# Performance work log

Measured on AMD Instinct MI355X. Metric: run time of the kernel, lower is better.

## Reference

```python
import jax, jax.numpy as jnp
import numpy as np

H, D = 8, 16
HD = H * D
SCALE0 = float(1.0 / np.sqrt(D * 1))   # degree-0 dot-product scale (order m=1)
SCALE1 = float(1.0 / np.sqrt(D * 3))   # degree-1 dot-product scale (order m=3)
SHARED = float(np.sqrt(0.5))           # shared_scale = sqrt(1/2) for DOT_PROD + SHARED
NEG = -1e9


def _split_heads_q(x):  # (b,n,HD,m) -> (b,H,n,D,m)
    b, n, _, m = x.shape
    return x.reshape(b, n, H, D, m).transpose(0, 2, 1, 3, 4)


def _split_heads_k(x):  # (b,n,N,HD,m) -> (b,H,n,N,D,m)
    b, n, N, _, m = x.shape
    return x.reshape(b, n, N, H, D, m).transpose(0, 3, 1, 2, 4, 5)


def _augment_kv(k, v, feats, W_self, null_k, null_v):
    # attend_self: VNLinear self key/value; use_null_kv: learned null tokens.
    b, n = feats.shape[:2]
    m = feats.shape[-1]
    skv = jnp.einsum('oc,bncm->bnom', W_self, feats)          # (b,n,2HD,m)
    sk, sv = jnp.split(skv, 2, axis=-2)
    sk = _split_heads_q(sk)[:, :, :, None]                     # (b,H,n,1,D,m)
    sv = _split_heads_q(sv)[:, :, :, None]
    nk = jnp.broadcast_to(null_k[None, :, None, None], (b, H, n, 1, D, m))
    nv = jnp.broadcast_to(null_v[None, :, None, None], (b, H, n, 1, D, m))
    k = jnp.concatenate([nk, sk, k], axis=3)                   # (b,H,n,2+N,D,m)
    v = jnp.concatenate([nv, sv, v], axis=3)
    return k, v


def _merge_heads(x):  # (b,H,n,D,m) -> (b,n,HD,m)
    b, _, n, _, m = x.shape
    return x.transpose(0, 2, 1, 3, 4).reshape(b, n, HD, m)


def _forward(q0, k0, v0, q1, k1, v1, feats0, feats1, edges,
             W_self_kv0, W_self_kv1, W_bias, self_bias, null_bias,
             null_k0, null_v0, null_k1, null_v1, head_weights1,
             W_out0, W_out1, neighbor_mask):
    b, n, N = edges.shape[:3]
    q0h, k0h, v0h = _split_heads_q(q0), _split_heads_k(k0), _split_heads_k(v0)
    q1h, k1h, v1h = _split_heads_q(q1), _split_heads_k(k1), _split_heads_k(v1)
    k0h, v0h = _augment_kv(k0h, v0h, feats0, W_self_kv0, null_k0, null_v0)
    k1h, v1h = _augment_kv(k1h, v1h, feats1, W_self_kv1, null_k1, null_v1)

    # pair bias for degree 0 (to_order==1); prepend null/self bias columns
    edge_bias = jnp.einsum('bnje,he->bhnj', edges, W_bias)     # (b,H,n,N)
    nb = jnp.broadcast_to(null_bias[None, :, None, None], (b, H, n, 1))
    sb = jnp.broadcast_to(self_bias[None, :, None, None], (b, H, n, 1))
    bias = jnp.concatenate([nb, sb, edge_bias], axis=-1)        # (b,H,n,2+N)

    sim0 = jnp.einsum('bhndm,bhnjdm->bhnj', q0h, k0h) * SCALE0 + bias
    w1 = jax.nn.softplus(head_weights1)                         # (1,H,1,1)
    sim1 = jnp.einsum('bhndm,bhnjdm->bhnj', q1h, k1h) * (SCALE1 * w1)

    total = (sim0 + sim1) * SHARED
    mask = jnp.concatenate(
        [jnp.ones((b, 1, n, 2), dtype=bool),                    # null + self always valid
         neighbor_mask[:, None]], axis=-1)
    total = jnp.where(mask, total, NEG)
    attn = jax.nn.softmax(total, axis=-1)                       # shared across degrees

    out0 = _merge_heads(jnp.einsum('bhnj,bhnjdm->bhndm', attn, v0h))
    out1 = _merge_heads(jnp.einsum('bhnj,bhnjdm->bhndm', attn, v1h))

    y0 = jnp.einsum('oc,bncm->bnom', W_out0, out0)              # FiberLinear deg 0
    y1 = jnp.einsum('oc,bncm->bnom', W_out1, out1)              # FiberLinear deg 1
    return y0, y1


def setup_inputs() -> dict:
    key = jax.random.key(0)
    ks = jax.random.split(key, 20)
    b, n, N, e = 1, 2048, 32, 32
    d0, d1 = 128, 64
    f = lambda k, s: jax.random.normal(k, s, dtype=jnp.float32) * 0.1
    return {
        'q0': f(ks[0], (b, n, HD, 1)), 'k0': f(ks[1], (b, n, N, HD, 1)), 'v0': f(ks[2], (b, n, N, HD, 1)),
        'q1': f(ks[3], (b, n, HD, 3)), 'k1': f(ks[4], (b, n, N, HD, 3)), 'v1': f(ks[5], (b, n, N, HD, 3)),
        'feats0': f(ks[6], (b, n, d0, 1)), 'feats1': f(ks[7], (b, n, d1, 3)),
        'edges': f(ks[8], (b, n, N, e)),
        'W_self_kv0': f(ks[9], (2 * HD, d0)), 'W_self_kv1': f(ks[10], (2 * HD, d1)),
        'W_bias': f(ks[11], (H, e)),
        'self_bias': jnp.zeros((H,), jnp.float32), 'null_bias': jnp.zeros((H,), jnp.float32),
        'null_k0': jnp.zeros((H, D, 1), jnp.float32), 'null_v0': jnp.zeros((H, D, 1), jnp.float32),
        'null_k1': jnp.zeros((H, D, 3), jnp.float32), 'null_v1': jnp.zeros((H, D, 3), jnp.float32),
        'head_weights1': jnp.full((1, H, 1, 1), float(np.log(np.e - 1.0)), jnp.float32),
        'W_out0': f(ks[12], (d0, HD)), 'W_out1': f(ks[13], (d1, HD)),
        'neighbor_mask': jax.random.uniform(ks[14], (b, n, N)) > 0.1,
    }


def reference(q0, k0, v0, q1, k1, v1, feats0, feats1, edges,
              W_self_kv0, W_self_kv1, W_bias, self_bias, null_bias,
              null_k0, null_v0, null_k1, null_v1, head_weights1,
              W_out0, W_out1, neighbor_mask):
    return _forward(q0, k0, v0, q1, k1, v1, feats0, feats1, edges,
                    W_self_kv0, W_self_kv1, W_bias, self_bias, null_bias,
                    null_k0, null_v0, null_k1, null_v1, head_weights1,
                    W_out0, W_out1, neighbor_mask)
```

## Files before the change

kernel.cpp:

```cpp
#include <hip/hip_runtime.h>

constexpr int kH  = 8;
constexpr int kD  = 16;
constexpr int kHD = 128;
constexpr int kN  = 32;
constexpr int kE  = 32;
constexpr int kD0 = 128;
constexpr int kD1 = 64;
constexpr int kP  = 4;
constexpr int kP3 = 2;
constexpr int kPP = 8;

constexpr float SCALE0   = 0.25f;
constexpr float SCALE1   = 0.14433756729740643f;
constexpr float SHARED_S = 0.70710678118654752f;
constexpr float NEGV     = -1e9f;


__global__ __launch_bounds__(256) void k1_selfkv(
    const float* __restrict__ q0, const float* __restrict__ q1,
    const float* __restrict__ feats0, const float* __restrict__ feats1,
    const float* __restrict__ Wskv0, const float* __restrict__ Wskv1,
    const float* __restrict__ self_bias, const float* __restrict__ null_bias,
    const float* __restrict__ nk0, const float* __restrict__ nk1,
    const float* __restrict__ hw1,
    float* __restrict__ ws_sc, float* __restrict__ ws_sv0, float* __restrict__ ws_sv1)
{
  const int i0 = blockIdx.x * kP;
  const int t  = threadIdx.x;
  __shared__ __align__(16) float f0s[kP][kD0];
  __shared__ __align__(16) float f1s[kP][kD1 * 3];
  __shared__ __align__(16) float q0s[kP][kHD];
  __shared__ __align__(16) float q1s[kP][kHD * 3];
  __shared__ float sk0L[kP][kHD];
  __shared__ float sk1L[kP][kHD * 3];
  __shared__ float w1s[kH];

  for (int u = t; u < kP * 32; u += 256) { int p = u >> 5, r = u & 31;
    ((float4*)f0s[p])[r] = ((const float4*)(feats0 + (size_t)(i0 + p) * kD0))[r]; }
  for (int u = t; u < kP * 48; u += 256) { int p = u / 48, r = u % 48;
    ((float4*)f1s[p])[r] = ((const float4*)(feats1 + (size_t)(i0 + p) * kD1 * 3))[r]; }
  for (int u = t; u < kP * 32; u += 256) { int p = u >> 5, r = u & 31;
    ((float4*)q0s[p])[r] = ((const float4*)(q0 + (size_t)(i0 + p) * kHD))[r]; }
  for (int u = t; u < kP * 96; u += 256) { int p = u / 96, r = u % 96;
    ((float4*)q1s[p])[r] = ((const float4*)(q1 + (size_t)(i0 + p) * kHD * 3))[r]; }
  if (t < kH) w1s[t] = log1pf(expf(hw1[t]));
  __syncthreads();

  float acc0[kP] = {};
  {
    const float4* wr = (const float4*)(Wskv0 + t * kD0);
    #pragma unroll
    for (int g = 0; g < 32; ++g) {
      float4 w = wr[g]; int c = g * 4;
      #pragma unroll
      for (int p = 0; p < kP; ++p)
        acc0[p] += w.x * f0s[p][c] + w.y * f0s[p][c + 1]
                 + w.z * f0s[p][c + 2] + w.w * f0s[p][c + 3];
    }
  }
  float acc1[kP][3] = {};
  {
    const float4* wr = (const float4*)(Wskv1 + t * kD1);
    #pragma unroll
    for (int g = 0; g < 16; ++g) {
      float4 w = wr[g]; int c = g * 4;
      float wv[4] = {w.x, w.y, w.z, w.w};
      #pragma unroll
      for (int q = 0; q < 4; ++q) {
        #pragma unroll
        for (int p = 0; p < kP; ++p) {
          const float* fp = &f1s[p][(c + q) * 3];
          acc1[p][0] += wv[q] * fp[0];
          acc1[p][1] += wv[q] * fp[1];
          acc1[p][2] += wv[q] * fp[2];
        }
      }
    }
  }
  if (t < kHD) {
    #pragma unroll
    for (int p = 0; p < kP; ++p) {
      sk0L[p][t] = acc0[p];
      sk1L[p][t * 3 + 0] = acc1[p][0];
      sk1L[p][t * 3 + 1] = acc1[p][1];
      sk1L[p][t * 3 + 2] = acc1[p][2];
    }
  } else {
    const int o = t - kHD;
    #pragma unroll
    for (int p = 0; p < kP; ++p) {
      ws_sv0[(size_t)(i0 + p) * kHD + o] = acc0[p];
      float* sp = ws_sv1 + (size_t)(i0 + p) * kHD * 3 + o * 3;
      sp[0] = acc1[p][0]; sp[1] = acc1[p][1]; sp[2] = acc1[p][2];
    }
  }
  __syncthreads();

  if (t < kP * 16) {
    const int p = t >> 4, idx = t & 15;
    const int h = idx & 7;
    const bool is_self = idx >= 8;
    float s0 = 0.f, s1 = 0.f, bias;
    if (is_self) {
      #pragma unroll
      for (int d = 0; d < kD; ++d) s0 += q0s[p][h * kD + d] * sk0L[p][h * kD + d];
      #pragma unroll
      for (int x = 0; x < 48; ++x) s1 += q1s[p][h * 48 + x] * sk1L[p][h * 48 + x];
      bias = self_bias[h];
    } else {
      #pragma unroll
      for (int d = 0; d < kD; ++d) s0 += q0s[p][h * kD + d] * nk0[h * kD + d];
      #pragma unroll
      for (int x = 0; x < 48; ++x) s1 += q1s[p][h * 48 + x] * nk1[h * 48 + x];
      bias = null_bias[h];
    }
    float total = (s0 * SCALE0 + bias + s1 * SCALE1 * w1s[h]) * SHARED_S;
    ws_sc[(size_t)(i0 + p) * 272 + h * 34 + (is_self ? 1 : 0)] = total;
  }
}

__global__ __launch_bounds__(256) void k2_sims(
    const float* __restrict__ q0, const float* __restrict__ q1,
    const float* __restrict__ k0, const float* __restrict__ k1,
    const float* __restrict__ edges, const float* __restrict__ Wbias,
    const float* __restrict__ hw1, const int* __restrict__ nmask,
    float* __restrict__ ws_sc)
{
  const int i = blockIdx.x;
  const int t = threadIdx.x;
  __shared__ __align__(16) float q0s[kHD];
  __shared__ __align__(16) float q1s[kHD * 3];
  __shared__ __align__(16) float edg[kN][kE + 1];
  __shared__ float wbs[kH * kE];
  __shared__ float w1s[kH];

  if (t < 32) {
    ((float4*)q0s)[t] = ((const float4*)(q0 + (size_t)i * kHD))[t];
  } else if (t < 128) {
    int r = t - 32;
    ((float4*)q1s)[r] = ((const float4*)(q1 + (size_t)i * kHD * 3))[r];
  }
  {
    float4 v = ((const float4*)(edges + (size_t)i * kN * kE))[t];
    int j = t >> 3, e4 = (t & 7) * 4;
    float* dst = &edg[j][e4];
    dst[0] = v.x; dst[1] = v.y; dst[2] = v.z; dst[3] = v.w;
  }
  if (t < kH * kE) wbs[t] = Wbias[t];
  if (t < kH) w1s[t] = log1pf(expf(hw1[t]));
  __syncthreads();

  const int h = t >> 5, j = t & 31;

  float bias = 0.f;
  #pragma unroll
  for (int e = 0; e < kE; ++e) bias += edg[j][e] * wbs[h * kE + e];

  float s0 = 0.f;
  const float4* kr0 = (const float4*)(k0 + ((size_t)i * kN + j) * kHD + h * kD);
  #pragma unroll
  for (int g = 0; g < 4; ++g) {
    float4 w = kr0[g]; int x = h * kD + g * 4;
    s0 += w.x * q0s[x] + w.y * q0s[x + 1] + w.z * q0s[x + 2] + w.w * q0s[x + 3];
  }
  float s1 = 0.f;
  const float4* kr1 = (const float4*)(k1 + ((size_t)i * kN + j) * kHD * 3 + h * 48);
  #pragma unroll
  for (int g = 0; g < 12; ++g) {
    float4 w = kr1[g]; int x = h * 48 + g * 4;
    s1 += w.x * q1s[x] + w.y * q1s[x + 1] + w.z * q1s[x + 2] + w.w * q1s[x + 3];
  }

  float total = (s0 * SCALE0 + bias + s1 * SCALE1 * w1s[h]) * SHARED_S;
  bool valid = nmask[(size_t)i * kN + j] != 0;
  float sc = valid ? total : NEGV;

  float* row = ws_sc + (size_t)i * 272 + h * 34;
  float e0v = row[0], e1v = row[1];

  float mx = sc;
  #pragma unroll
  for (int off = 16; off > 0; off >>= 1) mx = fmaxf(mx, __shfl_xor(mx, off));
  mx = fmaxf(mx, fmaxf(e0v, e1v));
  float ex = __expf(sc - mx);
  float sum = ex;
  #pragma unroll
  for (int off = 16; off > 0; off >>= 1) sum += __shfl_xor(sum, off);
  float ee0 = __expf(e0v - mx), ee1 = __expf(e1v - mx);
  float inv = 1.f / (sum + ee0 + ee1);

  row[2 + j] = ex * inv;
  if (j == 0) row[0] = ee0 * inv;
  if (j == 1) row[1] = ee1 * inv;
}

__global__ __launch_bounds__(256, 4) void k3_accum(
    const float* __restrict__ v0, const float* __restrict__ v1,
    const float* __restrict__ nv0, const float* __restrict__ nv1,
    const float* __restrict__ ws_sc,
    float* __restrict__ ws_sv0, float* __restrict__ ws_sv1)
{
  const int i0 = blockIdx.x * kP3;
  const int t  = threadIdx.x;
  __shared__ __align__(16) float attnL[kP3][272];

  if (t < kP3 * 68) {
    int p = t / 68, r = t % 68;
    ((float4*)attnL[p])[r] = ((const float4*)(ws_sc + (size_t)(i0 + p) * 272))[r];
  }
  __syncthreads();

  const int p = t >> 7, i = i0 + p;
  const int s = t & 127;
  float4 acc;
  if (s < 32) {
    const int h = s >> 2;
    const float* at = attnL[p] + h * 34;
    float4 nv = ((const float4*)nv0)[s];
    float4 sv = ((const float4*)(ws_sv0 + (size_t)i * kHD))[s];
    acc.x = at[0] * nv.x + at[1] * sv.x;
    acc.y = at[0] * nv.y + at[1] * sv.y;
    acc.z = at[0] * nv.z + at[1] * sv.z;
    acc.w = at[0] * nv.w + at[1] * sv.w;
    const float4* vp = (const float4*)(v0 + (size_t)i * kN * kHD) + s;
    float4 vbuf[8];
    #pragma unroll
    for (int g = 0; g < 4; ++g) {
      #pragma unroll
      for (int r = 0; r < 8; ++r) vbuf[r] = vp[(g * 8 + r) * 32];
      #pragma unroll
      for (int r = 0; r < 8; ++r) {
        float a = at[2 + g * 8 + r];
        acc.x += a * vbuf[r].x; acc.y += a * vbuf[r].y;
        acc.z += a * vbuf[r].z; acc.w += a * vbuf[r].w;
      }
    }
    ((float4*)(ws_sv0 + (size_t)i * kHD))[s] = acc;
  } else {
    const int s1 = s - 32;
    const int h = s1 / 12;
    const float* at = attnL[p] + h * 34;
    float4 nv = ((const float4*)nv1)[s1];
    float4 sv = ((const float4*)(ws_sv1 + (size_t)i * kHD * 3))[s1];
    acc.x = at[0] * nv.x + at[1] * sv.x;
    acc.y = at[0] * nv.y + at[1] * sv.y;
    acc.z = at[0] * nv.z + at[1] * sv.z;
    acc.w = at[0] * nv.w + at[1] * sv.w;
    const float4* vp = (const float4*)(v1 + (size_t)i * kN * kHD * 3) + s1;
    float4 vbuf[8];
    #pragma unroll
    for (int g = 0; g < 4; ++g) {
      #pragma unroll
      for (int r = 0; r < 8; ++r) vbuf[r] = vp[(g * 8 + r) * 96];
      #pragma unroll
      for (int r = 0; r < 8; ++r) {
        float a = at[2 + g * 8 + r];
        acc.x += a * vbuf[r].x; acc.y += a * vbuf[r].y;
        acc.z += a * vbuf[r].z; acc.w += a * vbuf[r].w;
      }
    }
    ((float4*)(ws_sv1 + (size_t)i * kHD * 3))[s1] = acc;
  }
}

__global__ __launch_bounds__(320) void k4_proj(
    const float* __restrict__ ws_o0, const float* __restrict__ ws_o1,
    const float* __restrict__ Wout0, const float* __restrict__ Wout1,
    float* __restrict__ out, int n_total)
{
  const int i0 = blockIdx.x * kPP;
  const int t  = threadIdx.x;
  __shared__ __align__(16) float o0L[kPP][kHD];
  __shared__ __align__(16) float o1L[kPP][kHD * 3];

  for (int u = t; u < kPP * 32; u += 320) { int p = u >> 5, r = u & 31;
    ((float4*)o0L[p])[r] = ((const float4*)(ws_o0 + (size_t)(i0 + p) * kHD))[r]; }
  for (int u = t; u < kPP * 96; u += 320) { int p = u / 96, r = u % 96;
    ((float4*)o1L[p])[r] = ((const float4*)(ws_o1 + (size_t)(i0 + p) * kHD * 3))[r]; }
  __syncthreads();

  if (t < 128) {
    float acc[kPP] = {};
    const float4* wr = (const float4*)(Wout0 + t * kHD);
    #pragma unroll
    for (int g = 0; g < 32; ++g) {
      float4 w = wr[g]; int c = g * 4;
      #pragma unroll
      for (int p = 0; p < kPP; ++p)
        acc[p] += w.x * o0L[p][c] + w.y * o0L[p][c + 1]
                + w.z * o0L[p][c + 2] + w.w * o0L[p][c + 3];
    }
    #pragma unroll
    for (int p = 0; p < kPP; ++p) out[(size_t)(i0 + p) * kHD + t] = acc[p];
  } else {
    const int v2 = t - 128, o = v2 / 3, m = v2 - o * 3;
    float acc[kPP] = {};
    const float4* wr = (const float4*)(Wout1 + o * kHD);
    #pragma unroll
    for (int g = 0; g < 32; ++g) {
      float4 w = wr[g]; int c = g * 4;
      #pragma unroll
      for (int p = 0; p < kPP; ++p)
        acc[p] += w.x * o1L[p][(c + 0) * 3 + m] + w.y * o1L[p][(c + 1) * 3 + m]
                + w.z * o1L[p][(c + 2) * 3 + m] + w.w * o1L[p][(c + 3) * 3 + m];
    }
    #pragma unroll
    for (int p = 0; p < kPP; ++p)
      out[(size_t)n_total * kHD + (size_t)(i0 + p) * 192 + v2] = acc[p];
  }
}

extern "C" void kernel_launch(void* const* d_in, const int* in_sizes, int n_in,
                              void* d_out, int out_size, void* d_ws, size_t ws_size,
                              hipStream_t stream) {
  const int n = in_sizes[0] / kHD;
  const float* q0     = (const float*)d_in[0];
  const float* k0     = (const float*)d_in[1];
  const float* v0     = (const float*)d_in[2];
  const float* q1     = (const float*)d_in[3];
  const float* k1     = (const float*)d_in[4];
  const float* v1     = (const float*)d_in[5];
  const float* feats0 = (const float*)d_in[6];
  const float* feats1 = (const float*)d_in[7];
  const float* edges  = (const float*)d_in[8];
  const float* Wskv0  = (const float*)d_in[9];
  const float* Wskv1  = (const float*)d_in[10];
  const float* Wbias  = (const float*)d_in[11];
  const float* sbias  = (const float*)d_in[12];
  const float* nbias  = (const float*)d_in[13];
  const float* nk0    = (const float*)d_in[14];
  const float* nv0    = (const float*)d_in[15];
  const float* nk1    = (const float*)d_in[16];
  const float* nv1    = (const float*)d_in[17];
  const float* hw1    = (const float*)d_in[18];
  const float* Wout0  = (const float*)d_in[19];
  const float* Wout1  = (const float*)d_in[20];
  const int*   nmask  = (const int*)d_in[21];

  float* ws     = (float*)d_ws;
  float* ws_sc  = ws;
  float* ws_sv0 = ws + (size_t)n * 272;
  float* ws_sv1 = ws + (size_t)n * 272 + (size_t)n * 128;

  k1_selfkv<<<n / kP, 256, 0, stream>>>(q0, q1, feats0, feats1, Wskv0, Wskv1,
                                        sbias, nbias, nk0, nk1, hw1,
                                        ws_sc, ws_sv0, ws_sv1);
  k2_sims<<<n, 256, 0, stream>>>(q0, q1, k0, k1, edges, Wbias, hw1, nmask, ws_sc);
  k3_accum<<<n / kP3, 256, 0, stream>>>(v0, v1, nv0, nv1, ws_sc, ws_sv0, ws_sv1);
  k4_proj<<<n / kPP, 320, 0, stream>>>(ws_sv0, ws_sv1, Wout0, Wout1, (float*)d_out, n);
}
```

Before: 364.0 us.

## Split each k2 score dot product across four lanes for coalesced key loads

Reworks the k2 score kernel so four adjacent lanes share one (head, neighbor) dot product, each loading one float4 slice of the k0/k1 rows and the edge bias. Partial sums are combined with shuffles and staged in shared memory, then a second phase does the per-head softmax as before. The aim is coalesced key-row reads with more loads in flight per thread, in place of each thread streaming a whole strided row. It adds an extra barrier, shared-memory staging and more registers, and sets a minimum-occupancy launch bound.

```diff
diff --git a/kernel.cpp b/kernel.cpp
--- a/kernel.cpp
+++ b/kernel.cpp
@@ -120,7 +120,7 @@
   }
 }
 
-__global__ __launch_bounds__(256) void k2_sims(
+__global__ __launch_bounds__(256, 4) void k2_sims(
     const float* __restrict__ q0, const float* __restrict__ q1,
     const float* __restrict__ k0, const float* __restrict__ k1,
     const float* __restrict__ edges, const float* __restrict__ Wbias,
@@ -134,6 +134,8 @@
   __shared__ __align__(16) float edg[kN][kE + 1];
   __shared__ float wbs[kH * kE];
   __shared__ float w1s[kH];
+  __shared__ float scL[kH][kN + 1];
+  __shared__ int   nmL[kN];
 
   if (t < 32) {
     ((float4*)q0s)[t] = ((const float4*)(q0 + (size_t)i * kHD))[t];
@@ -149,34 +151,63 @@
   }
   if (t < kH * kE) wbs[t] = Wbias[t];
   if (t < kH) w1s[t] = log1pf(expf(hw1[t]));
-  __syncthreads();
-
-  const int h = t >> 5, j = t & 31;
-
-  float bias = 0.f;
-  #pragma unroll
-  for (int e = 0; e < kE; ++e) bias += edg[j][e] * wbs[h * kE + e];
-
-  float s0 = 0.f;
-  const float4* kr0 = (const float4*)(k0 + ((size_t)i * kN + j) * kHD + h * kD);
-  #pragma unroll
-  for (int g = 0; g < 4; ++g) {
-    float4 w = kr0[g]; int x = h * kD + g * 4;
-    s0 += w.x * q0s[x] + w.y * q0s[x + 1] + w.z * q0s[x + 2] + w.w * q0s[x + 3];
-  }
-  float s1 = 0.f;
-  const float4* kr1 = (const float4*)(k1 + ((size_t)i * kN + j) * kHD * 3 + h * 48);
-  #pragma unroll
-  for (int g = 0; g < 12; ++g) {
-    float4 w = kr1[g]; int x = h * 48 + g * 4;
-    s1 += w.x * q1s[x] + w.y * q1s[x + 1] + w.z * q1s[x + 2] + w.w * q1s[x + 3];
-  }
-
-  float total = (s0 * SCALE0 + bias + s1 * SCALE1 * w1s[h]) * SHARED_S;
-  bool valid = nmask[(size_t)i * kN + j] != 0;
-  float sc = valid ? total : NEGV;
-
-  float* row = ws_sc + (size_t)i * 272 + h * 34;
+  if (t < kN) nmL[t] = nmask[(size_t)i * kN + t];
+  __syncthreads();
+
+  const int q  = t & 3;
+  const int m  = t >> 2;
+  const int h  = m & 7;
+  const int jl = m >> 3;
+  const float w1h = w1s[h];
+
+  const float4 q0f = *((const float4*)(q0s + h * kD) + q);
+  float4 q1f[3];
+  #pragma unroll
+  for (int pc = 0; pc < 3; ++pc)
+    q1f[pc] = *((const float4*)(q1s + h * 48 + pc * 16) + q);
+  float wbf[8];
+  #pragma unroll
+  for (int e = 0; e < 8; ++e) wbf[e] = wbs[h * kE + q * 8 + e];
+
+  const float* k0base = k0 + (size_t)i * kN * kHD + h * kD + q * 4;
+  const float* k1base = k1 + (size_t)i * kN * kHD * 3 + h * 48 + q * 4;
+
+  float4 kv0[4];
+  float4 kv1[4][3];
+  #pragma unroll
+  for (int p = 0; p < 4; ++p) {
+    const int j = p * 8 + jl;
+    kv0[p] = *((const float4*)(k0base + (size_t)j * kHD));
+    #pragma unroll
+    for (int pc = 0; pc < 3; ++pc)
+      kv1[p][pc] = *((const float4*)(k1base + (size_t)j * kHD * 3 + pc * 16));
+  }
+
+  #pragma unroll
+  for (int p = 0; p < 4; ++p) {
+    const int j = p * 8 + jl;
+    float s0 = kv0[p].x * q0f.x + kv0[p].y * q0f.y
+             + kv0[p].z * q0f.z + kv0[p].w * q0f.w;
+    float s1 = 0.f;
+    #pragma unroll
+    for (int pc = 0; pc < 3; ++pc)
+      s1 += kv1[p][pc].x * q1f[pc].x + kv1[p][pc].y * q1f[pc].y
+          + kv1[p][pc].z * q1f[pc].z + kv1[p][pc].w * q1f[pc].w;
+    float bias = 0.f;
+    #pragma unroll
+    for (int e = 0; e < 8; ++e) bias += edg[j][q * 8 + e] * wbf[e];
+
+    float part = s0 * SCALE0 + bias + s1 * SCALE1 * w1h;
+    part += __shfl_xor(part, 1);
+    part += __shfl_xor(part, 2);
+    float total = part * SHARED_S;
+    if (q == 0) scL[h][j] = nmL[j] ? total : NEGV;
+  }
+  __syncthreads();
+
+  const int hh = t >> 5, jj = t & 31;
+  float sc = scL[hh][jj];
+  float* row = ws_sc + (size_t)i * 272 + hh * 34;
   float e0v = row[0], e1v = row[1];
 
   float mx = sc;
@@ -190,9 +221,9 @@
   float ee0 = __expf(e0v - mx), ee1 = __expf(e1v - mx);
   float inv = 1.f / (sum + ee0 + ee1);
 
-  row[2 + j] = ex * inv;
-  if (j == 0) row[0] = ee0 * inv;
-  if (j == 1) row[1] = ee1 * inv;
+  row[2 + jj] = ex * inv;
+  if (jj == 0) row[0] = ee0 * inv;
+  if (jj == 1) row[1] = ee1 * inv;
 }
 
 __global__ __launch_bounds__(256, 4) void k3_accum(
```

New measurement: 349.9 us. 3.9% less time.
